# Optimization experiments

Hardware: AMD Instinct MI355X
Metric: run time of the kernel (lower is better)

The kernel has to match this reference:

```python
import jax, jax.numpy as jnp
import numpy as np

N_EMBD = 768
HEAD_SIZE = 64
B, T = 8, 4096


def setup_inputs() -> dict:
    key = jax.random.key(0)
    ks = jax.random.split(key, 7)
    s = 0.02  # small init scale for weights
    return {
        "x": jax.random.normal(ks[0], (B, T, N_EMBD), dtype=jnp.float32),
        "Wq": jax.random.normal(ks[1], (N_EMBD, HEAD_SIZE), dtype=jnp.float32) * s,
        "bq": jax.random.normal(ks[2], (HEAD_SIZE,), dtype=jnp.float32) * s,
        "Wk": jax.random.normal(ks[3], (N_EMBD, HEAD_SIZE), dtype=jnp.float32) * s,
        "bk": jax.random.normal(ks[4], (HEAD_SIZE,), dtype=jnp.float32) * s,
        "Wv": jax.random.normal(ks[5], (N_EMBD, HEAD_SIZE), dtype=jnp.float32) * s,
        "bv": jax.random.normal(ks[6], (HEAD_SIZE,), dtype=jnp.float32) * s,
    }


def reference(x, Wq, bq, Wk, bk, Wv, bv):
    # x: [B, T, C]; note: scale uses C = n_embd (input dim), per the original code.
    C = x.shape[-1]
    scale = jnp.asarray(C, x.dtype) ** -0.5
    q = x @ Wq + bq  # [B, T, H]
    k = x @ Wk + bk  # [B, T, H]
    v = x @ Wv + bv  # [B, T, H]
    wei = jnp.einsum("bqh,bkh->bqk", q, k) * scale  # [B, T, T]
    att = jax.nn.softmax(wei, axis=-1)
    # dropout p=0.0 (eval mode) -> identity
    out = jnp.einsum("bqk,bkh->bqh", att, v)  # [B, T, H]
    return out
```

## Files before the change

### kernel.cpp

```cpp
#include <hip/hip_runtime.h>
#include <stdint.h>

#define T_SEQ 4096
#define CEMB 768
#define HS 64

typedef __attribute__((ext_vector_type(8))) short bf16x8;
typedef __attribute__((ext_vector_type(16))) float f32x16;

__device__ __forceinline__ short bfru(float f) {
    uint32_t u = __builtin_bit_cast(uint32_t, f);
    return (short)((u + 0x8000u) >> 16);
}
__device__ __forceinline__ short bftr(float f) {
    return (short)(__builtin_bit_cast(uint32_t, f) >> 16);
}

#define QSCALE (0.036084391824351615f * 1.4426950408889634f)

__global__ __launch_bounds__(256) void prep_wt(const float* __restrict__ Wq,
                                               const float* __restrict__ Wk,
                                               const float* __restrict__ Wv,
                                               short* __restrict__ wtf) {
    const int p = blockIdx.x;
    const int ct = p / 48, kq = p % 48;
    const int tid = threadIdx.x;
    const int lane = tid & 63, jp = tid >> 6;
    const int l31 = lane & 31, lhi = lane >> 5;
    const int k = kq * 16 + lhi * 8 + jp * 2;
    const int nn = ct * 32 + l31;
    const float* W = nn < 64 ? Wq : (nn < 128 ? Wk : Wv);
    const int col = nn & 63;
    uint32_t lo = (uint16_t)bfru(W[k * 64 + col]);
    uint32_t hi = (uint16_t)bfru(W[(k + 1) * 64 + col]);
    *(uint32_t*)&wtf[(p * 64 + lane) * 8 + jp * 2] = lo | (hi << 16);
}

__global__ __launch_bounds__(256) void qkv_proj(const float* __restrict__ x,
        const float* __restrict__ bq, const float* __restrict__ bk, const float* __restrict__ bv,
        const short* __restrict__ wtf,
        short* __restrict__ qo, short* __restrict__ ko, short* __restrict__ vto) {
    __shared__ short S[64 * 72];

    const int tid  = threadIdx.x;
    const int wave = tid >> 6, lane = tid & 63;
    const int l31  = lane & 31, lhi = lane >> 5;
    const int rg   = wave & 1;
    const int ctb  = (wave >> 1) * 3;
    const int rowbase = blockIdx.x * 64;

    f32x16 acc[3];
    #pragma unroll
    for (int c = 0; c < 3; ++c) {
        const int ct = ctb + c, nn = ct * 32 + l31;
        const float bb = nn < 64 ? bq[nn] : (nn < 128 ? bk[nn - 64] : bv[nn - 128]);
        #pragma unroll
        for (int r = 0; r < 16; ++r) acc[c][r] = bb;
    }

    const int sr = tid >> 2, sseg = (tid & 3) * 16;
    for (int kt = 0; kt < 12; ++kt) {
        const float4* src = (const float4*)(x + (long)(rowbase + sr) * CEMB + kt * 64 + sseg);
        float4 f0 = src[0], f1 = src[1], f2 = src[2], f3 = src[3];
        bf16x8 w0, w1;
        w0[0]=bfru(f0.x); w0[1]=bfru(f0.y); w0[2]=bfru(f0.z); w0[3]=bfru(f0.w);
        w0[4]=bfru(f1.x); w0[5]=bfru(f1.y); w0[6]=bfru(f1.z); w0[7]=bfru(f1.w);
        w1[0]=bfru(f2.x); w1[1]=bfru(f2.y); w1[2]=bfru(f2.z); w1[3]=bfru(f2.w);
        w1[4]=bfru(f3.x); w1[5]=bfru(f3.y); w1[6]=bfru(f3.z); w1[7]=bfru(f3.w);
        *(bf16x8*)&S[sr * 72 + sseg]     = w0;
        *(bf16x8*)&S[sr * 72 + sseg + 8] = w1;
        __syncthreads();
        #pragma unroll
        for (int kc = 0; kc < 4; ++kc) {
            bf16x8 af = *(const bf16x8*)&S[(rg * 32 + l31) * 72 + kc * 16 + lhi * 8];
            #pragma unroll
            for (int c = 0; c < 3; ++c) {
                bf16x8 wf = *(const bf16x8*)&wtf[((ctb + c) * 48 + kt * 4 + kc) * 512 + lane * 8];
                acc[c] = __builtin_amdgcn_mfma_f32_32x32x16_bf16(af, wf, acc[c], 0, 0, 0);
            }
        }
        __syncthreads();
    }

    #pragma unroll
    for (int c = 0; c < 3; ++c) {
        const int ct = ctb + c;
        if (ct < 2) {
            #pragma unroll
            for (int r = 0; r < 16; ++r) {
                const int row = rg * 32 + (r & 3) + 8 * (r >> 2) + 4 * lhi;
                qo[(long)(rowbase + row) * HS + ct * 32 + l31] = bfru(acc[c][r] * QSCALE);
            }
        } else if (ct < 4) {
            #pragma unroll
            for (int r = 0; r < 16; ++r) {
                const int row = rg * 32 + (r & 3) + 8 * (r >> 2) + 4 * lhi;
                ko[(long)(rowbase + row) * HS + (ct - 2) * 32 + l31] = bfru(acc[c][r]);
            }
        } else {
            #pragma unroll
            for (int r = 0; r < 16; ++r) {
                const int row = rg * 32 + (r & 3) + 8 * (r >> 2) + 4 * lhi;
                S[((ct - 4) * 32 + l31) * 72 + row] = bfru(acc[c][r]);
            }
        }
    }
    __syncthreads();
    if (tid < 128) {
        const int vcol = tid >> 1, hh = tid & 1;
        const int b = rowbase >> 12, t0 = rowbase & 4095;
        short* dst = vto + ((long)b * HS + vcol) * T_SEQ + t0 + hh * 32;
        #pragma unroll
        for (int i = 0; i < 4; ++i)
            *(bf16x8*)(dst + i * 8) = *(const bf16x8*)&S[vcol * 72 + hh * 32 + i * 8];
    }
}

__global__ __launch_bounds__(256, 4) void attn(const short* __restrict__ qm,
        const short* __restrict__ km, const short* __restrict__ vtm,
        float* __restrict__ Op, float* __restrict__ lp, const int ks,
        float* __restrict__ outdirect) {
    __shared__ short Klds[64 * 72];
    __shared__ short Vlds[64 * 72];
    __shared__ short Plds[4][32 * 40];

    const int tid  = threadIdx.x;
    const int wave = tid >> 6, lane = tid & 63;
    const int l31  = lane & 31, lhi = lane >> 5;
    const int idx  = blockIdx.x;
    const int b = idx & 7, s = (idx >> 3) % ks, qt = idx / (8 * ks);
    const int slab = T_SEQ / ks, nkt = slab / 64;

    const short* qb = qm + ((long)b * T_SEQ + qt * 128) * HS;
    const short* kb = km + ((long)b * T_SEQ + s * slab) * HS;
    const short* vb = vtm + (long)b * HS * T_SEQ + s * slab;

    bf16x8 qf[4];
    #pragma unroll
    for (int kc = 0; kc < 4; ++kc)
        qf[kc] = *(const bf16x8*)&qb[(wave * 32 + l31) * HS + kc * 16 + lhi * 8];

    bf16x8 ones;
    #pragma unroll
    for (int j = 0; j < 8; ++j) ones[j] = (short)0x3F80;

    f32x16 oacc[2] = {};
    f32x16 lacc = {};
    short* pw = &Plds[wave][0];

    const int sr = tid >> 2, sc = (tid & 3) * 16;
    for (int kt = 0; kt < nkt; ++kt) {
        const int k0 = kt * 64;
        {   const short* p1 = &kb[(k0 + sr) * HS + sc];
            *(bf16x8*)&Klds[sr * 72 + sc]     = *(const bf16x8*)p1;
            *(bf16x8*)&Klds[sr * 72 + sc + 8] = *(const bf16x8*)(p1 + 8); }
        {   const short* p2 = &vb[sr * T_SEQ + k0 + sc];
            *(bf16x8*)&Vlds[sr * 72 + sc]     = *(const bf16x8*)p2;
            *(bf16x8*)&Vlds[sr * 72 + sc + 8] = *(const bf16x8*)(p2 + 8); }
        __syncthreads();

        #pragma unroll
        for (int ct = 0; ct < 2; ++ct) {
            f32x16 z = {};
            #pragma unroll
            for (int kc = 0; kc < 4; ++kc) {
                bf16x8 kf = *(const bf16x8*)&Klds[(ct * 32 + l31) * 72 + kc * 16 + lhi * 8];
                z = __builtin_amdgcn_mfma_f32_32x32x16_bf16(qf[kc], kf, z, 0, 0, 0);
            }
            #pragma unroll
            for (int r = 0; r < 16; ++r) {
                const int row = (r & 3) + 8 * (r >> 2) + 4 * lhi;
                pw[row * 40 + l31] = bftr(__builtin_amdgcn_exp2f(z[r]));
            }
            #pragma unroll
            for (int kc2 = 0; kc2 < 2; ++kc2) {
                bf16x8 pf = *(const bf16x8*)&pw[l31 * 40 + kc2 * 16 + lhi * 8];
                lacc = __builtin_amdgcn_mfma_f32_32x32x16_bf16(pf, ones, lacc, 0, 0, 0);
                #pragma unroll
                for (int ht = 0; ht < 2; ++ht) {
                    bf16x8 vf = *(const bf16x8*)&Vlds[(ht * 32 + l31) * 72 + ct * 32 + kc2 * 16 + lhi * 8];
                    oacc[ht] = __builtin_amdgcn_mfma_f32_32x32x16_bf16(pf, vf, oacc[ht], 0, 0, 0);
                }
            }
        }
        __syncthreads();
    }

    const long rowg = (long)b * T_SEQ + qt * 128 + wave * 32;
    if (outdirect) {
        float* ob = outdirect + rowg * HS;
        #pragma unroll
        for (int ht = 0; ht < 2; ++ht)
            #pragma unroll
            for (int r = 0; r < 16; ++r) {
                const int row = (r & 3) + 8 * (r >> 2) + 4 * lhi;
                ob[row * HS + ht * 32 + l31] = oacc[ht][r] / lacc[r];
            }
    } else {
        float* op = Op + ((long)s * 32768 + rowg) * HS;
        #pragma unroll
        for (int ht = 0; ht < 2; ++ht)
            #pragma unroll
            for (int r = 0; r < 16; ++r) {
                const int row = (r & 3) + 8 * (r >> 2) + 4 * lhi;
                op[row * HS + ht * 32 + l31] = oacc[ht][r];
            }
        if (l31 == 0) {
            #pragma unroll
            for (int r = 0; r < 16; ++r)
                lp[(long)s * 32768 + rowg + (r & 3) + 8 * (r >> 2) + 4 * lhi] = lacc[r];
        }
    }
}

__global__ __launch_bounds__(256) void combine(const float4* __restrict__ Op,
        const float* __restrict__ lp, float4* __restrict__ out, const int ks) {
    const int idx = blockIdx.x * 256 + threadIdx.x;
    const int row = idx >> 4, h4 = idx & 15;
    float ox = 0.f, oy = 0.f, oz = 0.f, ow = 0.f, l = 0.f;
    for (int s = 0; s < ks; ++s) {
        float4 t = Op[(long)(s * 32768 + row) * 16 + h4];
        ox += t.x; oy += t.y; oz += t.z; ow += t.w;
        l += lp[s * 32768 + row];
    }
    const float inv = 1.0f / l;
    float4 o; o.x = ox * inv; o.y = oy * inv; o.z = oz * inv; o.w = ow * inv;
    out[(long)row * 16 + h4] = o;
}

extern "C" void kernel_launch(void* const* d_in, const int* in_sizes, int n_in,
                              void* d_out, int out_size, void* d_ws, size_t ws_size,
                              hipStream_t stream) {
    const float* x  = (const float*)d_in[0];
    const float* Wq = (const float*)d_in[1];
    const float* bq = (const float*)d_in[2];
    const float* Wk = (const float*)d_in[3];
    const float* bk = (const float*)d_in[4];
    const float* Wv = (const float*)d_in[5];
    const float* bv = (const float*)d_in[6];

    char* ws = (char*)d_ws;
    short* qo  = (short*)(ws);
    short* ko  = (short*)(ws + (4u << 20));
    short* vto = (short*)(ws + (8u << 20));
    short* wtf = (short*)(ws + (12u << 20));
    const size_t opOff = 12582912u + 294912u;
    float* Op = (float*)(ws + opOff);

    const size_t per_s = 8388608u + 131072u;
    int ks = (ws_size >= opOff + 4 * per_s) ? 4
           : (ws_size >= opOff + 2 * per_s) ? 2 : 1;
    float* lp = (float*)(ws + opOff + (size_t)ks * 8388608u);

    prep_wt<<<288, 256, 0, stream>>>(Wq, Wk, Wv, wtf);
    qkv_proj<<<512, 256, 0, stream>>>(x, bq, bk, bv, wtf, qo, ko, vto);
    attn<<<256 * ks, 256, 0, stream>>>(qo, ko, vto, Op, lp, ks,
                                       ks == 1 ? (float*)d_out : nullptr);
    if (ks > 1)
        combine<<<2048, 256, 0, stream>>>((const float4*)Op, lp, (float4*)d_out, ks);
}
```

Before: 226.5 us.

## Restructure attention: transposed S, register P via permlane, double-buffered K/V, 64 rows per wave

The attention kernel now computes S transposed (K as the A operand), so each lane holds a column of P. P is converted with packed bf16 conversion and rearranged through v_permlane32_swap into the A-operand layout, which removes the per-wave LDS round trip for P. The row sum is now a VALU reduction plus a cross-half shuffle instead of an MFMA against a ones vector. Each wave handles 64 query rows (two 32-row subtiles) to reuse the K/V fragments it loads, and K/V tiles are double-buffered in LDS with register prefetch, leaving one barrier per tile. This raises register use (occupancy hint lowered to 2) and halves the grid. P now uses round-to-nearest bf16 conversion instead of truncation.

```diff
diff --git a/kernel.cpp b/kernel.cpp
--- a/kernel.cpp
+++ b/kernel.cpp
@@ -7,13 +7,16 @@
 
 typedef __attribute__((ext_vector_type(8))) short bf16x8;
 typedef __attribute__((ext_vector_type(16))) float f32x16;
+typedef __attribute__((ext_vector_type(4))) unsigned int u32x4;
 
 __device__ __forceinline__ short bfru(float f) {
     uint32_t u = __builtin_bit_cast(uint32_t, f);
     return (short)((u + 0x8000u) >> 16);
 }
-__device__ __forceinline__ short bftr(float f) {
-    return (short)(__builtin_bit_cast(uint32_t, f) >> 16);
+__device__ __forceinline__ uint32_t cvtpk_bf16(float lo, float hi) {
+    uint32_t r;
+    asm("v_cvt_pk_bf16_f32 %0, %1, %2" : "=v"(r) : "v"(lo), "v"(hi));
+    return r;
 }
 
 #define QSCALE (0.036084391824351615f * 1.4426950408889634f)
@@ -23,10 +26,10 @@
                                                const float* __restrict__ Wv,
                                                short* __restrict__ wtf) {
     const int p = blockIdx.x;
-    const int ct = p / 48, kq = p % 48;
     const int tid = threadIdx.x;
     const int lane = tid & 63, jp = tid >> 6;
     const int l31 = lane & 31, lhi = lane >> 5;
+    const int kq = p % 48, ct = p / 48;
     const int k = kq * 16 + lhi * 8 + jp * 2;
     const int nn = ct * 32 + l31;
     const float* W = nn < 64 ? Wq : (nn < 128 ? Wk : Wv);
@@ -116,13 +119,13 @@
     }
 }
 
-__global__ __launch_bounds__(256, 4) void attn(const short* __restrict__ qm,
+__global__ __launch_bounds__(256, 2) void attn(const short* __restrict__ qm,
         const short* __restrict__ km, const short* __restrict__ vtm,
         float* __restrict__ Op, float* __restrict__ lp, const int ks,
         float* __restrict__ outdirect) {
-    __shared__ short Klds[64 * 72];
-    __shared__ short Vlds[64 * 72];
-    __shared__ short Plds[4][32 * 40];
+    __shared__ short Klds[2][64 * 72];
+    __shared__ short Vlds[2][64 * 72];
+    __shared__ float Lred[4][2][32];
 
     const int tid  = threadIdx.x;
     const int wave = tid >> 6, lane = tid & 63;
@@ -131,84 +134,126 @@
     const int b = idx & 7, s = (idx >> 3) % ks, qt = idx / (8 * ks);
     const int slab = T_SEQ / ks, nkt = slab / 64;
 
-    const short* qb = qm + ((long)b * T_SEQ + qt * 128) * HS;
+    const short* qb = qm + ((long)b * T_SEQ + qt * 256 + wave * 64) * HS;
     const short* kb = km + ((long)b * T_SEQ + s * slab) * HS;
     const short* vb = vtm + (long)b * HS * T_SEQ + s * slab;
 
-    bf16x8 qf[4];
+    bf16x8 qf[2][4];
     #pragma unroll
-    for (int kc = 0; kc < 4; ++kc)
-        qf[kc] = *(const bf16x8*)&qb[(wave * 32 + l31) * HS + kc * 16 + lhi * 8];
-
-    bf16x8 ones;
+    for (int qs = 0; qs < 2; ++qs)
+        #pragma unroll
+        for (int kc = 0; kc < 4; ++kc)
+            qf[qs][kc] = *(const bf16x8*)&qb[(qs * 32 + l31) * HS + kc * 16 + lhi * 8];
+
+    f32x16 oacc[2][2] = {};
+    float lsum[2] = {0.f, 0.f};
+
+    const int sr = tid >> 2, sc = (tid & 3) * 16;
+    const short* kp = kb + sr * HS + sc;
+    const short* vp = vb + sr * T_SEQ + sc;
+
+    bf16x8 kr0 = *(const bf16x8*)kp, kr1 = *(const bf16x8*)(kp + 8);
+    bf16x8 vr0 = *(const bf16x8*)vp, vr1 = *(const bf16x8*)(vp + 8);
+    *(bf16x8*)&Klds[0][sr * 72 + sc]     = kr0;
+    *(bf16x8*)&Klds[0][sr * 72 + sc + 8] = kr1;
+    *(bf16x8*)&Vlds[0][sr * 72 + sc]     = vr0;
+    *(bf16x8*)&Vlds[0][sr * 72 + sc + 8] = vr1;
+    __syncthreads();
+
+    for (int kt = 0; kt < nkt; ++kt) {
+        const int cur = kt & 1;
+        const bool pfe = (kt + 1 < nkt);
+        if (pfe) {
+            const short* kp2 = kp + (kt + 1) * (64 * HS);
+            const short* vp2 = vp + (kt + 1) * 64;
+            kr0 = *(const bf16x8*)kp2; kr1 = *(const bf16x8*)(kp2 + 8);
+            vr0 = *(const bf16x8*)vp2; vr1 = *(const bf16x8*)(vp2 + 8);
+        }
+        const short* Kc = Klds[cur];
+        const short* Vc = Vlds[cur];
+        #pragma unroll
+        for (int ct = 0; ct < 2; ++ct) {
+            const short* krow = &Kc[(ct * 32 + l31) * 72 + lhi * 8];
+            bf16x8 kf0 = *(const bf16x8*)(krow);
+            bf16x8 kf1 = *(const bf16x8*)(krow + 16);
+            bf16x8 kf2 = *(const bf16x8*)(krow + 32);
+            bf16x8 kf3 = *(const bf16x8*)(krow + 48);
+            const short* vrow = &Vc[l31 * 72 + ct * 32 + lhi * 8];
+            bf16x8 vf00 = *(const bf16x8*)(vrow);
+            bf16x8 vf10 = *(const bf16x8*)(vrow + 16);
+            bf16x8 vf01 = *(const bf16x8*)(vrow + 32 * 72);
+            bf16x8 vf11 = *(const bf16x8*)(vrow + 32 * 72 + 16);
+            #pragma unroll
+            for (int qs = 0; qs < 2; ++qs) {
+                f32x16 z = {};
+                z = __builtin_amdgcn_mfma_f32_32x32x16_bf16(kf0, qf[qs][0], z, 0, 0, 0);
+                z = __builtin_amdgcn_mfma_f32_32x32x16_bf16(kf1, qf[qs][1], z, 0, 0, 0);
+                z = __builtin_amdgcn_mfma_f32_32x32x16_bf16(kf2, qf[qs][2], z, 0, 0, 0);
+                z = __builtin_amdgcn_mfma_f32_32x32x16_bf16(kf3, qf[qs][3], z, 0, 0, 0);
+                #pragma unroll
+                for (int r = 0; r < 16; ++r) z[r] = __builtin_amdgcn_exp2f(z[r]);
+                lsum[qs] += (((z[0]+z[1])+(z[2]+z[3])) + ((z[4]+z[5])+(z[6]+z[7])))
+                          + (((z[8]+z[9])+(z[10]+z[11])) + ((z[12]+z[13])+(z[14]+z[15])));
+                uint32_t x0 = cvtpk_bf16(z[0],  z[1]),  y0 = cvtpk_bf16(z[4],  z[5]);
+                uint32_t x1 = cvtpk_bf16(z[2],  z[3]),  y1 = cvtpk_bf16(z[6],  z[7]);
+                uint32_t x2 = cvtpk_bf16(z[8],  z[9]),  y2 = cvtpk_bf16(z[12], z[13]);
+                uint32_t x3 = cvtpk_bf16(z[10], z[11]), y3 = cvtpk_bf16(z[14], z[15]);
+                asm("v_permlane32_swap_b32 %0, %1" : "+v"(x0), "+v"(y0));
+                asm("v_permlane32_swap_b32 %0, %1" : "+v"(x1), "+v"(y1));
+                asm("v_permlane32_swap_b32 %0, %1" : "+v"(x2), "+v"(y2));
+                asm("v_permlane32_swap_b32 %0, %1" : "+v"(x3), "+v"(y3));
+                u32x4 t0 = {x0, x1, y0, y1};
+                u32x4 t1 = {x2, x3, y2, y3};
+                bf16x8 pa0 = __builtin_bit_cast(bf16x8, t0);
+                bf16x8 pa1 = __builtin_bit_cast(bf16x8, t1);
+                oacc[qs][0] = __builtin_amdgcn_mfma_f32_32x32x16_bf16(pa0, vf00, oacc[qs][0], 0, 0, 0);
+                oacc[qs][1] = __builtin_amdgcn_mfma_f32_32x32x16_bf16(pa0, vf01, oacc[qs][1], 0, 0, 0);
+                oacc[qs][0] = __builtin_amdgcn_mfma_f32_32x32x16_bf16(pa1, vf10, oacc[qs][0], 0, 0, 0);
+                oacc[qs][1] = __builtin_amdgcn_mfma_f32_32x32x16_bf16(pa1, vf11, oacc[qs][1], 0, 0, 0);
+            }
+        }
+        if (pfe) {
+            const int nxt = cur ^ 1;
+            *(bf16x8*)&Klds[nxt][sr * 72 + sc]     = kr0;
+            *(bf16x8*)&Klds[nxt][sr * 72 + sc + 8] = kr1;
+            *(bf16x8*)&Vlds[nxt][sr * 72 + sc]     = vr0;
+            *(bf16x8*)&Vlds[nxt][sr * 72 + sc + 8] = vr1;
+        }
+        __syncthreads();
+    }
+
     #pragma unroll
-    for (int j = 0; j < 8; ++j) ones[j] = (short)0x3F80;
-
-    f32x16 oacc[2] = {};
-    f32x16 lacc = {};
-    short* pw = &Plds[wave][0];
-
-    const int sr = tid >> 2, sc = (tid & 3) * 16;
-    for (int kt = 0; kt < nkt; ++kt) {
-        const int k0 = kt * 64;
-        {   const short* p1 = &kb[(k0 + sr) * HS + sc];
-            *(bf16x8*)&Klds[sr * 72 + sc]     = *(const bf16x8*)p1;
-            *(bf16x8*)&Klds[sr * 72 + sc + 8] = *(const bf16x8*)(p1 + 8); }
-        {   const short* p2 = &vb[sr * T_SEQ + k0 + sc];
-            *(bf16x8*)&Vlds[sr * 72 + sc]     = *(const bf16x8*)p2;
-            *(bf16x8*)&Vlds[sr * 72 + sc + 8] = *(const bf16x8*)(p2 + 8); }
+    for (int qs = 0; qs < 2; ++qs) lsum[qs] += __shfl_xor(lsum[qs], 32);
+
+    const long rowg = (long)b * T_SEQ + qt * 256 + wave * 64;
+    if (outdirect) {
+        if (lhi == 0) { Lred[wave][0][l31] = lsum[0]; Lred[wave][1][l31] = lsum[1]; }
         __syncthreads();
-
-        #pragma unroll
-        for (int ct = 0; ct < 2; ++ct) {
-            f32x16 z = {};
-            #pragma unroll
-            for (int kc = 0; kc < 4; ++kc) {
-                bf16x8 kf = *(const bf16x8*)&Klds[(ct * 32 + l31) * 72 + kc * 16 + lhi * 8];
-                z = __builtin_amdgcn_mfma_f32_32x32x16_bf16(qf[kc], kf, z, 0, 0, 0);
-            }
-            #pragma unroll
-            for (int r = 0; r < 16; ++r) {
-                const int row = (r & 3) + 8 * (r >> 2) + 4 * lhi;
-                pw[row * 40 + l31] = bftr(__builtin_amdgcn_exp2f(z[r]));
-            }
-            #pragma unroll
-            for (int kc2 = 0; kc2 < 2; ++kc2) {
-                bf16x8 pf = *(const bf16x8*)&pw[l31 * 40 + kc2 * 16 + lhi * 8];
-                lacc = __builtin_amdgcn_mfma_f32_32x32x16_bf16(pf, ones, lacc, 0, 0, 0);
+        float* ob = outdirect + rowg * HS;
+        #pragma unroll
+        for (int qs = 0; qs < 2; ++qs)
+            #pragma unroll
+            for (int ht = 0; ht < 2; ++ht)
                 #pragma unroll
-                for (int ht = 0; ht < 2; ++ht) {
-                    bf16x8 vf = *(const bf16x8*)&Vlds[(ht * 32 + l31) * 72 + ct * 32 + kc2 * 16 + lhi * 8];
-                    oacc[ht] = __builtin_amdgcn_mfma_f32_32x32x16_bf16(pf, vf, oacc[ht], 0, 0, 0);
+                for (int r = 0; r < 16; ++r) {
+                    const int row = (r & 3) + 8 * (r >> 2) + 4 * lhi;
+                    ob[(long)(qs * 32 + row) * HS + ht * 32 + l31] =
+                        oacc[qs][ht][r] / Lred[wave][qs][row];
                 }
-            }
-        }
-        __syncthreads();
-    }
-
-    const long rowg = (long)b * T_SEQ + qt * 128 + wave * 32;
-    if (outdirect) {
-        float* ob = outdirect + rowg * HS;
-        #pragma unroll
-        for (int ht = 0; ht < 2; ++ht)
-            #pragma unroll
-            for (int r = 0; r < 16; ++r) {
-                const int row = (r & 3) + 8 * (r >> 2) + 4 * lhi;
-                ob[row * HS + ht * 32 + l31] = oacc[ht][r] / lacc[r];
-            }
     } else {
         float* op = Op + ((long)s * 32768 + rowg) * HS;
         #pragma unroll
-        for (int ht = 0; ht < 2; ++ht)
-            #pragma unroll
-            for (int r = 0; r < 16; ++r) {
-                const int row = (r & 3) + 8 * (r >> 2) + 4 * lhi;
-                op[row * HS + ht * 32 + l31] = oacc[ht][r];
-            }
-        if (l31 == 0) {
-            #pragma unroll
-            for (int r = 0; r < 16; ++r)
-                lp[(long)s * 32768 + rowg + (r & 3) + 8 * (r >> 2) + 4 * lhi] = lacc[r];
+        for (int qs = 0; qs < 2; ++qs)
+            #pragma unroll
+            for (int ht = 0; ht < 2; ++ht)
+                #pragma unroll
+                for (int r = 0; r < 16; ++r) {
+                    const int row = (r & 3) + 8 * (r >> 2) + 4 * lhi;
+                    op[(qs * 32 + row) * HS + ht * 32 + l31] = oacc[qs][ht][r];
+                }
+        if (lhi == 0) {
+            lp[(long)s * 32768 + rowg + l31]      = lsum[0];
+            lp[(long)s * 32768 + rowg + 32 + l31] = lsum[1];
         }
     }
 }
@@ -254,7 +299,7 @@
 
     prep_wt<<<288, 256, 0, stream>>>(Wq, Wk, Wv, wtf);
     qkv_proj<<<512, 256, 0, stream>>>(x, bq, bk, bv, wtf, qo, ko, vto);
-    attn<<<256 * ks, 256, 0, stream>>>(qo, ko, vto, Op, lp, ks,
+    attn<<<128 * ks, 256, 0, stream>>>(qo, ko, vto, Op, lp, ks,
                                        ks == 1 ? (float*)d_out : nullptr);
     if (ks > 1)
         combine<<<2048, 256, 0, stream>>>((const float4*)Op, lp, (float4*)d_out, ks);
```

New measurement: 217.4 us. 4.0% less time.
